# Optimization experiments

Measured on AMD Instinct MI355X. Metric: run time of the kernel, lower is better.

## Reference

```python
import jax, jax.numpy as jnp
import numpy as np

D_MODEL = 1024
HEADS = 16
D_K = 64
B, S = 2, 2048


def setup_inputs() -> dict:
    key = jax.random.key(0)
    ks = jax.random.split(key, 12)
    s = 0.02
    return {
        "query": jax.random.normal(ks[0], (B, S, D_MODEL), dtype=jnp.float32),
        "key": jax.random.normal(ks[1], (B, S, D_MODEL), dtype=jnp.float32),
        "value": jax.random.normal(ks[2], (B, S, D_MODEL), dtype=jnp.float32),
        "Wq": jax.random.normal(ks[3], (D_MODEL, HEADS * D_K), dtype=jnp.float32) * s,
        "bq": jnp.zeros((HEADS * D_K,), dtype=jnp.float32),
        "Wk": jax.random.normal(ks[4], (D_MODEL, HEADS * D_K), dtype=jnp.float32) * s,
        "bk": jnp.zeros((HEADS * D_K,), dtype=jnp.float32),
        "Wv": jax.random.normal(ks[5], (D_MODEL, HEADS * D_K), dtype=jnp.float32) * s,
        "bv": jnp.zeros((HEADS * D_K,), dtype=jnp.float32),
        "Wo": jax.random.normal(ks[6], (HEADS * D_K, D_MODEL), dtype=jnp.float32) * s,
        "bo": jnp.zeros((D_MODEL,), dtype=jnp.float32),
    }


def reference(query, key, value, Wq, bq, Wk, bk, Wv, bv, Wo, bo):
    b, s, _ = query.shape
    scale = 1.0 / np.sqrt(D_K).astype(np.float32)
    # project and split heads: [b, s, h, d_k]
    q = (query @ Wq + bq).reshape(b, s, HEADS, D_K)
    k = (key @ Wk + bk).reshape(b, s, HEADS, D_K)
    v = (value @ Wv + bv).reshape(b, s, HEADS, D_K)
    # attention scores [b, i, j, h]
    scores = jnp.einsum('bihd,bjhd->bijh', q, k) * scale
    # NOTE: original uses nn.Softmax(dim=1) -> normalize over query axis i (faithful quirk)
    attn = jax.nn.softmax(scores, axis=1)
    # dropout is identity in eval mode
    x = jnp.einsum('bijh,bjhd->bihd', attn, v).reshape(b, s, HEADS * D_K)
    return x @ Wo + bo
```

## Files before the change

### kernel.cpp

```cpp
#include <hip/hip_runtime.h>
#include <hip/hip_bf16.h>

#define SEQ   2048
#define NH    16
#define DK    64
#define DM    1024
#define NTOK  4096
#define C1    0.1803368801111204f

typedef unsigned short u16;
typedef unsigned int   u32;
typedef short bhalf8 __attribute__((ext_vector_type(8)));
typedef float floatx4 __attribute__((ext_vector_type(4)));

#define MFMA16(a,b,c) __builtin_amdgcn_mfma_f32_16x16x32_bf16(a,b,c,0,0,0)

#if __has_builtin(__builtin_amdgcn_exp2f)
#define EXP2(x) __builtin_amdgcn_exp2f(x)
#else
#define EXP2(x) exp2f(x)
#endif

__device__ __forceinline__ u16 f2b(float f){
  union { float f; u32 u; } v; v.f = f;
  u32 r = v.u + 0x7fffu + ((v.u >> 16) & 1u);
  return (u16)(r >> 16);
}
__device__ __forceinline__ u32 pk2(float a, float b){
  union { __hip_bfloat162 h; u32 w; } o;
  o.h = __float22bfloat162_rn(make_float2(a, b));
  return o.w;
}
__device__ __forceinline__ void gld_lds16(const u16* g, u16* lds){
  __builtin_amdgcn_global_load_lds(
      (const __attribute__((address_space(1))) u32*)g,
      (__attribute__((address_space(3))) u32*)lds, 16, 0, 0);
}

__global__ __launch_bounds__(256)
void cvt_qkv(const float* __restrict__ q, const float* __restrict__ k,
             const float* __restrict__ v, u16* __restrict__ Aq,
             u16* __restrict__ Ak, u16* __restrict__ Av)
{
  const float* in = (blockIdx.y == 0) ? q : (blockIdx.y == 1) ? k : v;
  u16* out       = (blockIdx.y == 0) ? Aq : (blockIdx.y == 1) ? Ak : Av;
  const size_t i = ((size_t)blockIdx.x * 256 + threadIdx.x) * 8;
  const float4 a = *(const float4*)(in + i);
  const float4 b = *(const float4*)(in + i + 4);
  uint4 o;
  o.x = pk2(a.x, a.y); o.y = pk2(a.z, a.w);
  o.z = pk2(b.x, b.y); o.w = pk2(b.z, b.w);
  *(uint4*)(out + i) = o;
}

__global__ __launch_bounds__(256)
void wtrans4(const float* __restrict__ Wq, const float* __restrict__ Wk,
             const float* __restrict__ Wv, const float* __restrict__ Wo,
             u16* __restrict__ Wtall)
{
  __shared__ __align__(16) u16 T[64][68];
  const int z = blockIdx.z;
  const float* W = (z == 0) ? Wq : (z == 1) ? Wk : (z == 2) ? Wv : Wo;
  u16* Wt = Wtall + (size_t)z * DM * DM;
  const int k0 = blockIdx.y * 64, n0 = blockIdx.x * 64;
  const int t = threadIdx.x;
  #pragma unroll
  for (int p = 0; p < 16; ++p){
    int e = p*256 + t, k = e >> 6, n = e & 63;
    T[n][k] = f2b(W[(size_t)(k0+k)*DM + n0 + n]);
  }
  __syncthreads();
  #pragma unroll
  for (int p = 0; p < 8; ++p){
    int e = p*256 + t, n = e >> 5, kp = e & 31;
    u32 val = *(const u32*)&T[n][2*kp];
    *(u32*)&Wt[(size_t)(n0+n)*DM + k0 + 2*kp] = val;
  }
}

__global__ __launch_bounds__(256)
void gemm_qkv(const u16* __restrict__ Aq, const u16* __restrict__ Ak,
              const u16* __restrict__ Av, const u16* __restrict__ Wtall,
              const float* __restrict__ bq, const float* __restrict__ bk,
              const float* __restrict__ bv, u16* __restrict__ Qb,
              u16* __restrict__ Kb, u16* __restrict__ Vt)
{
  __shared__ __align__(16) u16 Asm[2][128*32];
  __shared__ __align__(16) u16 Bsm[2][128*32];
  const int z = blockIdx.z;
  const u16* A = (z == 0) ? Aq : (z == 1) ? Ak : Av;
  const u16* Wt = Wtall + (size_t)z * DM * DM;
  const float* bias = (z == 0) ? bq : (z == 1) ? bk : bv;
  const float cmul = (z == 0) ? C1 : 1.0f;

  const int bm = blockIdx.y * 128, bn = blockIdx.x * 128;
  const int t = threadIdx.x, wid = t >> 6, l = t & 63, r16 = l & 15, q = l >> 4;
  const int wm = (wid & 1) * 64, wn = (wid >> 1) * 64;
  const int rL = t >> 2, gL = ((t & 3) ^ (rL & 3)) * 8;
  const u16* Ag = A  + (size_t)(bm + rL)*DM + gL;
  const u16* Bg = Wt + (size_t)(bn + rL)*DM + gL;
  const int wo = wid*512;
  const int sw = (r16 & 3);
  floatx4 acc[4][4] = {};

  gld_lds16(Ag,                  Asm[0] + wo);
  gld_lds16(Ag + (size_t)64*DM,  Asm[0] + wo + 2048);
  gld_lds16(Bg,                  Bsm[0] + wo);
  gld_lds16(Bg + (size_t)64*DM,  Bsm[0] + wo + 2048);
  __syncthreads();

  int cur = 0;
  for (int kc = 0; kc < DM; kc += 32){
    if (kc + 32 < DM){
      const int nx = cur ^ 1;
      gld_lds16(Ag + kc + 32,                 Asm[nx] + wo);
      gld_lds16(Ag + kc + 32 + (size_t)64*DM, Asm[nx] + wo + 2048);
      gld_lds16(Bg + kc + 32,                 Bsm[nx] + wo);
      gld_lds16(Bg + kc + 32 + (size_t)64*DM, Bsm[nx] + wo + 2048);
    }
    __builtin_amdgcn_s_setprio(1);
    bhalf8 af[4], bf[4];
    #pragma unroll
    for (int i = 0; i < 4; ++i)
      af[i] = *(const bhalf8*)&Asm[cur][(wm + i*16 + r16)*32 + ((q ^ sw)*8)];
    #pragma unroll
    for (int j = 0; j < 4; ++j)
      bf[j] = *(const bhalf8*)&Bsm[cur][(wn + j*16 + r16)*32 + ((q ^ sw)*8)];
    #pragma unroll
    for (int i = 0; i < 4; ++i)
      #pragma unroll
      for (int j = 0; j < 4; ++j)
        acc[i][j] = MFMA16(af[i], bf[j], acc[i][j]);
    __builtin_amdgcn_s_setprio(0);
    __syncthreads();
    cur ^= 1;
  }

  if (z < 2){
    u16* C = (z == 0) ? Qb : Kb;
    #pragma unroll
    for (int j = 0; j < 4; ++j){
      const int n = bn + wn + j*16 + r16;
      const float bj = bias[n];
      #pragma unroll
      for (int i = 0; i < 4; ++i){
        const int m0 = bm + wm + i*16 + q*4;
        #pragma unroll
        for (int r = 0; r < 4; ++r)
          C[(size_t)(m0+r)*DM + n] = f2b((acc[i][j][r] + bj) * cmul);
      }
    }
  } else {
    const int h  = (bn + wn) >> 6;
    const int bb = (bm + wm) >> 11;
    const int s0 = (bm + wm) & (SEQ - 1);
    #pragma unroll
    for (int i = 0; i < 4; ++i){
      const int sl = s0 + i*16 + q*4;
      #pragma unroll
      for (int j = 0; j < 4; ++j){
        const int d = j*16 + r16;
        const float bj = bias[h*DK + d];
        u32 v0 = pk2(acc[i][j][0]+bj, acc[i][j][1]+bj);
        u32 v1 = pk2(acc[i][j][2]+bj, acc[i][j][3]+bj);
        *(uint2*)&Vt[((size_t)(bb*NH + h)*DK + d)*SEQ + sl] = make_uint2(v0, v1);
      }
    }
  }
}

__global__ __launch_bounds__(256)
void gemm_o(const u16* __restrict__ A, const u16* __restrict__ Wt,
            const float* __restrict__ bias, float* __restrict__ C)
{
  __shared__ __align__(16) u16 Asm[2][128*32];
  __shared__ __align__(16) u16 Bsm[2][128*32];
  const int bm = blockIdx.y * 128, bn = blockIdx.x * 128;
  const int t = threadIdx.x, wid = t >> 6, l = t & 63, r16 = l & 15, q = l >> 4;
  const int wm = (wid & 1) * 64, wn = (wid >> 1) * 64;
  const int rL = t >> 2, gL = ((t & 3) ^ (rL & 3)) * 8;
  const u16* Ag = A  + (size_t)(bm + rL)*DM + gL;
  const u16* Bg = Wt + (size_t)(bn + rL)*DM + gL;
  const int wo = wid*512;
  const int sw = (r16 & 3);
  floatx4 acc[4][4] = {};

  gld_lds16(Ag,                  Asm[0] + wo);
  gld_lds16(Ag + (size_t)64*DM,  Asm[0] + wo + 2048);
  gld_lds16(Bg,                  Bsm[0] + wo);
  gld_lds16(Bg + (size_t)64*DM,  Bsm[0] + wo + 2048);
  __syncthreads();

  int cur = 0;
  for (int kc = 0; kc < DM; kc += 32){
    if (kc + 32 < DM){
      const int nx = cur ^ 1;
      gld_lds16(Ag + kc + 32,                 Asm[nx] + wo);
      gld_lds16(Ag + kc + 32 + (size_t)64*DM, Asm[nx] + wo + 2048);
      gld_lds16(Bg + kc + 32,                 Bsm[nx] + wo);
      gld_lds16(Bg + kc + 32 + (size_t)64*DM, Bsm[nx] + wo + 2048);
    }
    __builtin_amdgcn_s_setprio(1);
    bhalf8 af[4], bf[4];
    #pragma unroll
    for (int i = 0; i < 4; ++i)
      af[i] = *(const bhalf8*)&Asm[cur][(wm + i*16 + r16)*32 + ((q ^ sw)*8)];
    #pragma unroll
    for (int j = 0; j < 4; ++j)
      bf[j] = *(const bhalf8*)&Bsm[cur][(wn + j*16 + r16)*32 + ((q ^ sw)*8)];
    #pragma unroll
    for (int i = 0; i < 4; ++i)
      #pragma unroll
      for (int j = 0; j < 4; ++j)
        acc[i][j] = MFMA16(af[i], bf[j], acc[i][j]);
    __builtin_amdgcn_s_setprio(0);
    __syncthreads();
    cur ^= 1;
  }
  #pragma unroll
  for (int j = 0; j < 4; ++j){
    const int n = bn + wn + j*16 + r16;
    const float bj = bias[n];
    #pragma unroll
    for (int i = 0; i < 4; ++i){
      const int m0 = bm + wm + i*16 + q*4;
      #pragma unroll
      for (int r = 0; r < 4; ++r)
        C[(size_t)(m0+r)*DM + n] = acc[i][j][r] + bj;
    }
  }
}

__global__ __launch_bounds__(256)
void attn_stats(const u16* __restrict__ Qb, const u16* __restrict__ Kb,
                u16* __restrict__ Vt)
{
  __shared__ float pl[4][64];
  __shared__ float sLinv[64];
  const int j0 = blockIdx.x * 64, bh = blockIdx.y, b = bh >> 4, h = bh & 15;
  const int t = threadIdx.x, wid = t >> 6, l = t & 63, r16 = l & 15, q = l >> 4;

  bhalf8 kf[4][2];
  const u16* kp = Kb + (size_t)(b*SEQ + j0 + r16)*DM + h*DK + q*8;
  #pragma unroll
  for (int st = 0; st < 4; ++st){
    kf[st][0] = *(const bhalf8*)(kp + (size_t)st*16*DM);
    kf[st][1] = *(const bhalf8*)(kp + (size_t)st*16*DM + 32);
  }
  float rl[4] = {0.f, 0.f, 0.f, 0.f};
  const u16* qp = Qb + (size_t)(b*SEQ + wid*16 + r16)*DM + h*DK + q*8;
  for (int it = 0; it < SEQ/64; ++it){
    bhalf8 qf0 = *(const bhalf8*)qp;
    bhalf8 qf1 = *(const bhalf8*)(qp + 32);
    qp += (size_t)64*DM;
    #pragma unroll
    for (int st = 0; st < 4; ++st){
      floatx4 s = {};
      s = MFMA16(qf0, kf[st][0], s);
      s = MFMA16(qf1, kf[st][1], s);
      rl[st] += EXP2(s[0]) + EXP2(s[1]) + EXP2(s[2]) + EXP2(s[3]);
    }
  }
  #pragma unroll
  for (int st = 0; st < 4; ++st){
    float v = rl[st];
    v += __shfl_xor(v, 16);
    v += __shfl_xor(v, 32);
    rl[st] = v;
  }
  if (q == 0){
    #pragma unroll
    for (int st = 0; st < 4; ++st) pl[wid][st*16 + r16] = rl[st];
  }
  __syncthreads();
  if (t < 64)
    sLinv[t] = 1.f / (pl[0][t] + pl[1][t] + pl[2][t] + pl[3][t]);
  __syncthreads();
  {
    const int d = t >> 2, cb = (t & 3) * 16;
    u16* vp = Vt + ((size_t)bh*DK + d)*SEQ + j0 + cb;
    uint4 w0 = *(uint4*)vp, w1 = *(uint4*)(vp + 8);
    float sc[16];
    #pragma unroll
    for (int e = 0; e < 16; ++e) sc[e] = sLinv[cb + e];
    #define SC2(w, s0, s1) pk2(__uint_as_float((w) << 16) * (s0), \
                               __uint_as_float((w) & 0xffff0000u) * (s1))
    w0.x = SC2(w0.x, sc[0],  sc[1]);  w0.y = SC2(w0.y, sc[2],  sc[3]);
    w0.z = SC2(w0.z, sc[4],  sc[5]);  w0.w = SC2(w0.w, sc[6],  sc[7]);
    w1.x = SC2(w1.x, sc[8],  sc[9]);  w1.y = SC2(w1.y, sc[10], sc[11]);
    w1.z = SC2(w1.z, sc[12], sc[13]); w1.w = SC2(w1.w, sc[14], sc[15]);
    #undef SC2
    *(uint4*)vp = w0; *(uint4*)(vp + 8) = w1;
  }
}

__global__ __launch_bounds__(256)
void attn_pv(const u16* __restrict__ Qb, const u16* __restrict__ Kb,
             const u16* __restrict__ Vt, u16* __restrict__ Xb)
{
  __shared__ __align__(16) u16 Kls[2][64*64];
  __shared__ __align__(16) u16 Vls[2][64*64];
  __shared__ __align__(16) u16 Pls[4][32][72];
  const int i0 = blockIdx.x * 128, bh = blockIdx.y, b = bh >> 4, h = bh & 15;
  const int t = threadIdx.x, wid = t >> 6, l = t & 63, r16 = l & 15, q = l >> 4;

  bhalf8 qf[2][2];
  #pragma unroll
  for (int g = 0; g < 2; ++g){
    const u16* qp = Qb + (size_t)(b*SEQ + i0 + wid*32 + g*16 + r16)*DM + h*DK + q*8;
    qf[g][0] = *(const bhalf8*)qp;
    qf[g][1] = *(const bhalf8*)(qp + 32);
  }

  const int row0 = t >> 3, c0 = t & 7;
  const int g0 = (c0 ^ (row0 & 7)) * 8;
  const int row1 = row0 + 32;
  const int g1 = (c0 ^ (row1 & 7)) * 8;
  const u16* kp0 = Kb + (size_t)(b*SEQ + row0)*DM + h*DK + g0;
  const u16* kp1 = Kb + (size_t)(b*SEQ + row1)*DM + h*DK + g1;
  const u16* vp0 = Vt + ((size_t)bh*DK + row0)*SEQ + g0;
  const u16* vp1 = Vt + ((size_t)bh*DK + row1)*SEQ + g1;
  const int wo = wid*512;
  const int sw = (r16 & 7);

  floatx4 xacc[2][4] = {};

  gld_lds16(kp0, &Kls[0][wo]);
  gld_lds16(kp1, &Kls[0][wo + 2048]);
  gld_lds16(vp0, &Vls[0][wo]);
  gld_lds16(vp1, &Vls[0][wo + 2048]);
  __syncthreads();

  int cur = 0;
  for (int jt = 0; jt < SEQ/64; ++jt){
    if (jt + 1 < SEQ/64){
      const int nx = cur ^ 1;
      gld_lds16(kp0 + (size_t)(jt+1)*64*DM, &Kls[nx][wo]);
      gld_lds16(kp1 + (size_t)(jt+1)*64*DM, &Kls[nx][wo + 2048]);
      gld_lds16(vp0 + (jt+1)*64,            &Vls[nx][wo]);
      gld_lds16(vp1 + (jt+1)*64,            &Vls[nx][wo + 2048]);
    }
    const u16* Kc = &Kls[cur][0];
    const u16* Vc = &Vls[cur][0];

    __builtin_amdgcn_s_setprio(1);
    bhalf8 vf[4][2];
    #pragma unroll
    for (int dst = 0; dst < 4; ++dst){
      const int vr = (dst*16 + r16) * 64;
      vf[dst][0] = *(const bhalf8*)&Vc[vr + ((q     ^ sw) * 8)];
      vf[dst][1] = *(const bhalf8*)&Vc[vr + (((q+4) ^ sw) * 8)];
    }

    #pragma unroll
    for (int st = 0; st < 4; ++st){
      const int kr = (st*16 + r16) * 64;
      bhalf8 k0 = *(const bhalf8*)&Kc[kr + ((q     ^ sw) * 8)];
      bhalf8 k1 = *(const bhalf8*)&Kc[kr + (((q+4) ^ sw) * 8)];
      #pragma unroll
      for (int g = 0; g < 2; ++g){
        floatx4 s = {};
        s = MFMA16(k0, qf[g][0], s);
        s = MFMA16(k1, qf[g][1], s);
        u32 lo = pk2(EXP2(s[0]), EXP2(s[1]));
        u32 hi = pk2(EXP2(s[2]), EXP2(s[3]));
        *(uint2*)&Pls[wid][g*16 + r16][st*16 + q*4] = make_uint2(lo, hi);
      }
    }
    #pragma unroll
    for (int g = 0; g < 2; ++g){
      bhalf8 pf0 = *(const bhalf8*)&Pls[wid][g*16 + r16][q*8];
      bhalf8 pf1 = *(const bhalf8*)&Pls[wid][g*16 + r16][32 + q*8];
      #pragma unroll
      for (int dst = 0; dst < 4; ++dst){
        xacc[g][dst] = MFMA16(pf0, vf[dst][0], xacc[g][dst]);
        xacc[g][dst] = MFMA16(pf1, vf[dst][1], xacc[g][dst]);
      }
    }
    __builtin_amdgcn_s_setprio(0);
    __syncthreads();
    cur ^= 1;
  }

  #pragma unroll
  for (int g = 0; g < 2; ++g)
    #pragma unroll
    for (int dst = 0; dst < 4; ++dst)
      #pragma unroll
      for (int r = 0; r < 4; ++r)
        Xb[(size_t)(b*SEQ + i0 + wid*32 + g*16 + q*4 + r)*DM + h*DK + dst*16 + r16]
          = f2b(xacc[g][dst][r]);
}

extern "C" void kernel_launch(void* const* d_in, const int* in_sizes, int n_in,
                              void* d_out, int out_size, void* d_ws, size_t ws_size,
                              hipStream_t stream)
{
  const float* q  = (const float*)d_in[0];
  const float* k  = (const float*)d_in[1];
  const float* v  = (const float*)d_in[2];
  const float* Wq = (const float*)d_in[3];
  const float* bq = (const float*)d_in[4];
  const float* Wk = (const float*)d_in[5];
  const float* bk = (const float*)d_in[6];
  const float* Wv = (const float*)d_in[7];
  const float* bv = (const float*)d_in[8];
  const float* Wo = (const float*)d_in[9];
  const float* bo = (const float*)d_in[10];
  float* out = (float*)d_out;

  char* ws = (char*)d_ws;
  const size_t WTB  = (size_t)DM * DM * sizeof(u16);
  const size_t TOKB = (size_t)NTOK * DM * sizeof(u16);
  u16* Wtall = (u16*)(ws);
  u16* Aq    = (u16*)(ws + 4*WTB);
  u16* Ak    = (u16*)(ws + 4*WTB + TOKB);
  u16* Av    = (u16*)(ws + 4*WTB + 2*TOKB);
  u16* Qb    = (u16*)(ws + 4*WTB + 3*TOKB);
  u16* Kb    = (u16*)(ws + 4*WTB + 4*TOKB);
  u16* Vt    = (u16*)(ws + 4*WTB + 5*TOKB);
  u16* Xb    = Aq;

  dim3 blk(256);
  cvt_qkv<<<dim3((NTOK*DM)/(256*8), 3), blk, 0, stream>>>(q, k, v, Aq, Ak, Av);
  wtrans4<<<dim3(16, 16, 4), blk, 0, stream>>>(Wq, Wk, Wv, Wo, Wtall);
  gemm_qkv<<<dim3(DM/128, NTOK/128, 3), blk, 0, stream>>>(
      Aq, Ak, Av, Wtall, bq, bk, bv, Qb, Kb, Vt);
  attn_stats<<<dim3(SEQ/64, NH*2), blk, 0, stream>>>(Qb, Kb, Vt);
  attn_pv<<<dim3(SEQ/128, NH*2), blk, 0, stream>>>(Qb, Kb, Vt, Xb);
  gemm_o<<<dim3(DM/128, NTOK/128), blk, 0, stream>>>(
      Xb, Wtall + 3*(size_t)DM*DM, bo, out);
}
```

Before: 262.0 us.

## Keep softmax P tile in registers and compute transposed PV with 16x16x16 MFMA

Removes the per-wave LDS staging buffer for the exponentiated score tile. The P fragments now stay in registers as the B operand of 16x16x16 bf16 MFMAs, which compute X transposed from V rows read straight out of LDS. This drops an LDS write/read round trip and the matching shared memory footprint per iteration. In exchange it issues twice as many smaller MFMAs with narrower V loads, and the output store is rewritten to pack pairs of bf16 values for the transposed accumulator layout.

```diff
diff --git a/kernel.cpp b/kernel.cpp
--- a/kernel.cpp
+++ b/kernel.cpp
@@ -11,9 +11,11 @@
 typedef unsigned short u16;
 typedef unsigned int   u32;
 typedef short bhalf8 __attribute__((ext_vector_type(8)));
+typedef short bhalf4 __attribute__((ext_vector_type(4)));
 typedef float floatx4 __attribute__((ext_vector_type(4)));
 
 #define MFMA16(a,b,c) __builtin_amdgcn_mfma_f32_16x16x32_bf16(a,b,c,0,0,0)
+#define MFMA4(a,b,c)  __builtin_amdgcn_mfma_f32_16x16x16bf16_1k(a,b,c,0,0,0)
 
 #if __has_builtin(__builtin_amdgcn_exp2f)
 #define EXP2(x) __builtin_amdgcn_exp2f(x)
@@ -300,7 +302,6 @@
 {
   __shared__ __align__(16) u16 Kls[2][64*64];
   __shared__ __align__(16) u16 Vls[2][64*64];
-  __shared__ __align__(16) u16 Pls[4][32][72];
   const int i0 = blockIdx.x * 128, bh = blockIdx.y, b = bh >> 4, h = bh & 15;
   const int t = threadIdx.x, wid = t >> 6, l = t & 63, r16 = l & 15, q = l >> 4;
 
@@ -323,7 +324,7 @@
   const int wo = wid*512;
   const int sw = (r16 & 7);
 
-  floatx4 xacc[2][4] = {};
+  floatx4 xaccT[2][4] = {};
 
   gld_lds16(kp0, &Kls[0][wo]);
   gld_lds16(kp1, &Kls[0][wo + 2048]);
@@ -344,14 +345,7 @@
     const u16* Vc = &Vls[cur][0];
 
     __builtin_amdgcn_s_setprio(1);
-    bhalf8 vf[4][2];
-    #pragma unroll
-    for (int dst = 0; dst < 4; ++dst){
-      const int vr = (dst*16 + r16) * 64;
-      vf[dst][0] = *(const bhalf8*)&Vc[vr + ((q     ^ sw) * 8)];
-      vf[dst][1] = *(const bhalf8*)&Vc[vr + (((q+4) ^ sw) * 8)];
-    }
-
+    bhalf4 pb[4][2];
     #pragma unroll
     for (int st = 0; st < 4; ++st){
       const int kr = (st*16 + r16) * 64;
@@ -362,20 +356,25 @@
         floatx4 s = {};
         s = MFMA16(k0, qf[g][0], s);
         s = MFMA16(k1, qf[g][1], s);
-        u32 lo = pk2(EXP2(s[0]), EXP2(s[1]));
-        u32 hi = pk2(EXP2(s[2]), EXP2(s[3]));
-        *(uint2*)&Pls[wid][g*16 + r16][st*16 + q*4] = make_uint2(lo, hi);
+        union { uint2 u; bhalf4 h; } pu;
+        pu.u = make_uint2(pk2(EXP2(s[0]), EXP2(s[1])),
+                          pk2(EXP2(s[2]), EXP2(s[3])));
+        pb[st][g] = pu.h;
       }
     }
     #pragma unroll
-    for (int g = 0; g < 2; ++g){
-      bhalf8 pf0 = *(const bhalf8*)&Pls[wid][g*16 + r16][q*8];
-      bhalf8 pf1 = *(const bhalf8*)&Pls[wid][g*16 + r16][32 + q*8];
-      #pragma unroll
-      for (int dst = 0; dst < 4; ++dst){
-        xacc[g][dst] = MFMA16(pf0, vf[dst][0], xacc[g][dst]);
-        xacc[g][dst] = MFMA16(pf1, vf[dst][1], xacc[g][dst]);
+    for (int dst = 0; dst < 4; ++dst){
+      bhalf4 va[4];
+      #pragma unroll
+      for (int st = 0; st < 4; ++st){
+        const int ch = (st*2 + (q >> 1)) ^ (r16 & 7);
+        va[st] = *(const bhalf4*)&Vc[(dst*16 + r16)*64 + ch*8 + (q & 1)*4];
       }
+      #pragma unroll
+      for (int g = 0; g < 2; ++g)
+        #pragma unroll
+        for (int st = 0; st < 4; ++st)
+          xaccT[g][dst] = MFMA4(va[st], pb[st][g], xaccT[g][dst]);
     }
     __builtin_amdgcn_s_setprio(0);
     __syncthreads();
@@ -383,13 +382,15 @@
   }
 
   #pragma unroll
-  for (int g = 0; g < 2; ++g)
-    #pragma unroll
-    for (int dst = 0; dst < 4; ++dst)
-      #pragma unroll
-      for (int r = 0; r < 4; ++r)
-        Xb[(size_t)(b*SEQ + i0 + wid*32 + g*16 + q*4 + r)*DM + h*DK + dst*16 + r16]
-          = f2b(xacc[g][dst][r]);
+  for (int g = 0; g < 2; ++g){
+    const size_t irow = (size_t)(b*SEQ + i0 + wid*32 + g*16 + r16);
+    #pragma unroll
+    for (int dst = 0; dst < 4; ++dst){
+      u32 w0 = (u32)f2b(xaccT[g][dst][0]) | ((u32)f2b(xaccT[g][dst][1]) << 16);
+      u32 w1 = (u32)f2b(xaccT[g][dst][2]) | ((u32)f2b(xaccT[g][dst][3]) << 16);
+      *(uint2*)&Xb[irow*DM + h*DK + dst*16 + q*4] = make_uint2(w0, w1);
+    }
+  }
 }
 
 extern "C" void kernel_launch(void* const* d_in, const int* in_sizes, int n_in,
```

New measurement: 269.0 us. 1.03x slower.
